# Kernel tuning notes

Measured on AMD Instinct MI355X. Metric: run time of the kernel, lower is better.

## Reference

```python
import jax, jax.numpy as jnp
import numpy as np

IN_FEATURES = 4096
OUT_FEATURES = 11008
BLOCK_SIZE = 64
BITS = 4
RANGE_MAX = 2 ** (BITS - 1) - 1  # 7


def setup_inputs() -> dict:
    key = jax.random.key(0)
    k1, k2, k3, k4 = jax.random.split(key, 4)
    n_blocks = OUT_FEATURES * IN_FEATURES // BLOCK_SIZE
    x = jax.random.normal(k1, (4, 2048, IN_FEATURES), dtype=jnp.float32)
    # int4 codes in [-7, 7]; stored signed int. Use randint in [-7, 8).
    weight_quant = jax.random.randint(k2, (n_blocks, BLOCK_SIZE), -RANGE_MAX, RANGE_MAX + 1, dtype=jnp.int32)
    weight_absmax = jax.random.uniform(k3, (n_blocks, 1), dtype=jnp.float32, minval=1e-5, maxval=1.0)
    bias = jax.random.normal(k4, (OUT_FEATURES,), dtype=jnp.float32)
    return {"x": x, "weight_quant": weight_quant, "weight_absmax": weight_absmax, "bias": bias}


def reference(x, weight_quant, weight_absmax, bias):
    # Blockwise dequant: q/range_max * absmax per block, reshape to (out, in). padding=0.
    w = (weight_quant.astype(jnp.float32) / RANGE_MAX) * weight_absmax  # [n_blocks, block]
    w = w.reshape(OUT_FEATURES, IN_FEATURES)
    # F.linear: y = x @ W^T + b
    return jnp.einsum('bsi,oi->bso', x, w) + bias
```

## Files before the change

### kernel.cpp

```cpp
#include <hip/hip_runtime.h>


#define K_DIM 4096
#define N_DIM 11008
#define M_DIM 8192
#define NT_K 64
#define AB_OFF 98304

typedef _Float16 f16;
typedef _Float16 f16x8 __attribute__((ext_vector_type(8)));
typedef float f32x4 __attribute__((ext_vector_type(4)));
typedef float fv4 __attribute__((ext_vector_type(4)));
typedef int iv4 __attribute__((ext_vector_type(4)));

__device__ __forceinline__ void gload16(const void* g, void* lds) {
  __builtin_amdgcn_global_load_lds(
      (__attribute__((address_space(1))) void*)g,
      (__attribute__((address_space(3))) void*)lds,
      16, 0, 0);
}

__global__ __launch_bounds__(256) void prep_kernel(const float* __restrict__ x,
                                                   f16* __restrict__ xo, int n8x,
                                                   const int* __restrict__ q,
                                                   const float* __restrict__ amax,
                                                   f16* __restrict__ wo, int n8w) {
  int i = blockIdx.x * blockDim.x + threadIdx.x;
  if (i < n8x) {
    const fv4* xv = (const fv4*)x;
    fv4 a = __builtin_nontemporal_load(xv + 2 * (size_t)i);
    fv4 b = __builtin_nontemporal_load(xv + 2 * (size_t)i + 1);
    f16x8 o;
    o[0] = (f16)a.x; o[1] = (f16)a.y; o[2] = (f16)a.z; o[3] = (f16)a.w;
    o[4] = (f16)b.x; o[5] = (f16)b.y; o[6] = (f16)b.z; o[7] = (f16)b.w;
    *(f16x8*)(xo + (size_t)i * 8) = o;
  } else {
    int j = i - n8x;
    if (j >= n8w) return;
    const iv4* qv = (const iv4*)q;
    iv4 a = __builtin_nontemporal_load(qv + 2 * (size_t)j);
    iv4 b = __builtin_nontemporal_load(qv + 2 * (size_t)j + 1);
    float s = amax[j >> 3] * (1.0f / 7.0f);
    f16x8 o;
    o[0] = (f16)((float)a.x * s); o[1] = (f16)((float)a.y * s);
    o[2] = (f16)((float)a.z * s); o[3] = (f16)((float)a.w * s);
    o[4] = (f16)((float)b.x * s); o[5] = (f16)((float)b.y * s);
    o[6] = (f16)((float)b.z * s); o[7] = (f16)((float)b.w * s);
    *(f16x8*)(wo + (size_t)j * 8) = o;
  }
}

__global__ __launch_bounds__(512, 2) void gemm_f16_bt(const f16* __restrict__ A,
                                                      const f16* __restrict__ B,
                                                      const float* __restrict__ bias,
                                                      float* __restrict__ C) {
  __shared__ __align__(16) char lds[163840];

  const int tid = threadIdx.x;
  const int w = tid >> 6;
  const int l = tid & 63;
  const int wr = w >> 2;
  const int wc = w & 3;

  const int wg = blockIdx.x;
  const int swz = (wg & 7) * 172 + (wg >> 3);
  const int mt = swz / 43;
  const int nt = swz % 43;
  const int m0 = mt * 256;
  const int n0 = nt * 256;

  const int lr = l & 15;
  const int g = l >> 4;
  const int laneoff = ((lr >> 1) << 7) | (((((lr & 1) << 6) | (g << 4))) ^ (((lr >> 1) & 7) << 4));

  const char* Asrc[2];
  const char* Bsrc[2];
#pragma unroll
  for (int j = 0; j < 2; ++j) {
    const int u = ((j * 8 + w) << 10) + l * 16;
    const int r = u >> 7;
    const int cp = (u & 127) ^ ((r & 7) << 4);
    const int ra = 2 * r + (cp >> 6);
    const int kb = cp & 63;
    Asrc[j] = (const char*)A + (size_t)(m0 + ra) * (K_DIM * 2) + kb;
    Bsrc[j] = (const char*)B + (size_t)(n0 + ra) * (K_DIM * 2) + kb;
  }

  char* ldsc = (char*)lds;

#define STAGE_A(dst_off, koff)              \
  {                                         \
    char* d_ = ldsc + (dst_off) + w * 1024; \
    gload16(Asrc[0] + (koff), d_);          \
    gload16(Asrc[1] + (koff), d_ + 8192);   \
  }
#define STAGE_B(dst_off, koff)              \
  {                                         \
    char* d_ = ldsc + (dst_off) + w * 1024; \
    gload16(Bsrc[0] + (koff), d_);          \
    gload16(Bsrc[1] + (koff), d_ + 8192);   \
  }

  f32x4 acc[8][4];
#pragma unroll
  for (int i = 0; i < 8; ++i)
#pragma unroll
    for (int j = 0; j < 4; ++j) acc[i][j] = (f32x4){0.f, 0.f, 0.f, 0.f};

  STAGE_A(0, 0);
  STAGE_A(16384, 64);
  STAGE_B(AB_OFF, 0);
  STAGE_B(AB_OFF + 16384, 64);
  STAGE_A(32768, 128);
  STAGE_A(32768 + 16384, 192);
  STAGE_B(AB_OFF + 32768, 128);
  STAGE_B(AB_OFF + 32768 + 16384, 192);
  asm volatile("s_waitcnt vmcnt(8)" ::: "memory");
  __builtin_amdgcn_s_barrier();

  int ap = 0;
  int ap2 = 65536;

  for (int t = 0; t < NT_K; ++t) {
    const int p = t & 1;
    const int Bb = AB_OFF + p * 32768;
    const int t2 = (t + 2 < NT_K) ? (t + 2) : (NT_K - 1);
    const int k2 = t2 * 128;

    f16x8 bf[4];
    f16x8 af[4];
#pragma unroll
    for (int pi = 0; pi < 4; ++pi) {
      const int kk = pi >> 1;
      const int mh = pi & 1;

      if (mh == 0) {
#pragma unroll
        for (int ni = 0; ni < 4; ++ni)
          bf[ni] = *(const f16x8*)(ldsc + Bb + kk * 16384 + ((wc * 64 + ni * 16) << 6) + laneoff);
      }
#pragma unroll
      for (int mi = 0; mi < 4; ++mi)
        af[mi] = *(const f16x8*)(ldsc + ap + kk * 16384 +
                                 ((wr * 128 + mh * 64 + mi * 16) << 6) + laneoff);

      if (pi == 0) {
        STAGE_A(ap2, k2);
      } else if (pi == 1) {
        STAGE_A(ap2 + 16384, k2 + 64);
      } else if (pi == 2) {
        STAGE_B(Bb, k2);
      } else {
        STAGE_B(Bb + 16384, k2 + 64);
      }

      __builtin_amdgcn_s_barrier();
      __builtin_amdgcn_s_setprio(1);
#pragma unroll
      for (int mi = 0; mi < 4; ++mi)
#pragma unroll
        for (int ni = 0; ni < 4; ++ni)
          acc[mh * 4 + mi][ni] = __builtin_amdgcn_mfma_f32_16x16x32_f16(
              af[mi], bf[ni], acc[mh * 4 + mi][ni], 0, 0, 0);
      __builtin_amdgcn_s_setprio(0);
      if (pi == 3) asm volatile("s_waitcnt vmcnt(8)" ::: "memory");
      __builtin_amdgcn_s_barrier();
    }

    ap += 32768;  if (ap == AB_OFF) ap = 0;
    ap2 += 32768; if (ap2 == AB_OFF) ap2 = 0;
  }

  const int orow = g * 4;
  float bv[4];
#pragma unroll
  for (int ni = 0; ni < 4; ++ni) bv[ni] = bias[n0 + wc * 64 + ni * 16 + lr];
#pragma unroll
  for (int mi = 0; mi < 8; ++mi) {
    const int row = m0 + wr * 128 + mi * 16 + orow;
#pragma unroll
    for (int ni = 0; ni < 4; ++ni) {
      const size_t cb = (size_t)row * N_DIM + (n0 + wc * 64 + ni * 16 + lr);
#pragma unroll
      for (int j = 0; j < 4; ++j)
        __builtin_nontemporal_store(acc[mi][ni][j] + bv[ni], &C[cb + (size_t)j * N_DIM]);
    }
  }
#undef STAGE_A
#undef STAGE_B
}

extern "C" void kernel_launch(void* const* d_in, const int* in_sizes, int n_in,
                              void* d_out, int out_size, void* d_ws, size_t ws_size,
                              hipStream_t stream) {
  const float* x = (const float*)d_in[0];
  const int* wq = (const int*)d_in[1];
  const float* amax = (const float*)d_in[2];
  const float* bias = (const float*)d_in[3];
  float* out = (float*)d_out;

  f16* Xh = (f16*)d_ws;
  f16* Wh = (f16*)((char*)d_ws + (size_t)M_DIM * K_DIM * 2);

  {
    int n8x = M_DIM * K_DIM / 8;
    int n8w = N_DIM * K_DIM / 8;
    int nthr = n8x + n8w;
    prep_kernel<<<(nthr + 255) / 256, 256, 0, stream>>>(x, Xh, n8x, wq, amax, Wh, n8w);
  }
  {
    dim3 grid((M_DIM / 256) * (N_DIM / 256));
    gemm_f16_bt<<<grid, 512, 0, stream>>>(Xh, Wh, bias, out);
  }
}
```

Before: 769.2 us.

## Switch GEMM to 32x32x16 MFMA with 3-slot K-pipeline and register double-buffering

Rewrites the main GEMM loop to use 32x32x16 f16 MFMA instructions instead of 16x16x32, with a single 64-wide K step per iteration and a triple-buffered LDS ring (96KB instead of 160KB). Fragment loads for the next half-step are issued before the current MFMAs, so LDS reads overlap matrix math, and each iteration needs only one barrier instead of eight. Larger MFMA tiles cut the number of LDS fragment reads per FLOP. In exchange the prefetch distance is shorter in bytes, which makes the kernel more exposed to global-load latency, and the epilogue uses a different store pattern.

```diff
diff --git a/kernel.cpp b/kernel.cpp
--- a/kernel.cpp
+++ b/kernel.cpp
@@ -4,12 +4,11 @@
 #define K_DIM 4096
 #define N_DIM 11008
 #define M_DIM 8192
-#define NT_K 64
-#define AB_OFF 98304
+#define NT 128
 
 typedef _Float16 f16;
 typedef _Float16 f16x8 __attribute__((ext_vector_type(8)));
-typedef float f32x4 __attribute__((ext_vector_type(4)));
+typedef float f32x16 __attribute__((ext_vector_type(16)));
 typedef float fv4 __attribute__((ext_vector_type(4)));
 typedef int iv4 __attribute__((ext_vector_type(4)));
 
@@ -54,7 +53,7 @@
                                                       const f16* __restrict__ B,
                                                       const float* __restrict__ bias,
                                                       float* __restrict__ C) {
-  __shared__ __align__(16) char lds[163840];
+  __shared__ __align__(16) char lds[98304];
 
   const int tid = threadIdx.x;
   const int w = tid >> 6;
@@ -69,121 +68,127 @@
   const int m0 = mt * 256;
   const int n0 = nt * 256;
 
-  const int lr = l & 15;
-  const int g = l >> 4;
-  const int laneoff = ((lr >> 1) << 7) | (((((lr & 1) << 6) | (g << 4))) ^ (((lr >> 1) & 7) << 4));
-
-  const char* Asrc[2];
-  const char* Bsrc[2];
+  const int l31 = l & 31;
+  const int lbase = (l31 >> 1) << 7;
+  const int lxor = ((l31 >> 1) & 7) << 4;
+  const int lk = ((l & 1) << 6) | ((l >> 5) << 4);
+  const int lt0 = lk ^ lxor;
+  const int lt1 = (lk | 32) ^ lxor;
+
+  const char* AsrcP[2];
+  const char* BsrcP[2];
 #pragma unroll
   for (int j = 0; j < 2; ++j) {
-    const int u = ((j * 8 + w) << 10) + l * 16;
+    const int u = ((w + j * 8) << 10) + l * 16;
     const int r = u >> 7;
     const int cp = (u & 127) ^ ((r & 7) << 4);
     const int ra = 2 * r + (cp >> 6);
     const int kb = cp & 63;
-    Asrc[j] = (const char*)A + (size_t)(m0 + ra) * (K_DIM * 2) + kb;
-    Bsrc[j] = (const char*)B + (size_t)(n0 + ra) * (K_DIM * 2) + kb;
+    AsrcP[j] = (const char*)A + (size_t)(m0 + ra) * (K_DIM * 2) + kb;
+    BsrcP[j] = (const char*)B + (size_t)(n0 + ra) * (K_DIM * 2) + kb;
   }
 
   char* ldsc = (char*)lds;
 
-#define STAGE_A(dst_off, koff)              \
-  {                                         \
-    char* d_ = ldsc + (dst_off) + w * 1024; \
-    gload16(Asrc[0] + (koff), d_);          \
-    gload16(Asrc[1] + (koff), d_ + 8192);   \
-  }
-#define STAGE_B(dst_off, koff)              \
-  {                                         \
-    char* d_ = ldsc + (dst_off) + w * 1024; \
-    gload16(Bsrc[0] + (koff), d_);          \
-    gload16(Bsrc[1] + (koff), d_ + 8192);   \
-  }
-
-  f32x4 acc[8][4];
-#pragma unroll
-  for (int i = 0; i < 8; ++i)
-#pragma unroll
-    for (int j = 0; j < 4; ++j) acc[i][j] = (f32x4){0.f, 0.f, 0.f, 0.f};
+#define STAGE_A(slot, koff)                          \
+  {                                                  \
+    char* d_ = ldsc + (slot) + w * 1024;             \
+    gload16(AsrcP[0] + (koff), d_);                  \
+    gload16(AsrcP[1] + (koff), d_ + 8192);           \
+  }
+#define STAGE_B(slot, koff)                          \
+  {                                                  \
+    char* d_ = ldsc + (slot) + w * 1024;             \
+    gload16(BsrcP[0] + (koff), d_);                  \
+    gload16(BsrcP[1] + (koff), d_ + 8192);           \
+  }
+
+  f32x16 acc[4][2];
+#pragma unroll
+  for (int i = 0; i < 4; ++i)
+#pragma unroll
+    for (int j = 0; j < 2; ++j) acc[i][j] = (f32x16)0.f;
+
+  const int aW = wr * 8192;
+  const int bW = wc * 4096;
 
   STAGE_A(0, 0);
+  STAGE_B(49152, 0);
   STAGE_A(16384, 64);
-  STAGE_B(AB_OFF, 0);
-  STAGE_B(AB_OFF + 16384, 64);
-  STAGE_A(32768, 128);
-  STAGE_A(32768 + 16384, 192);
-  STAGE_B(AB_OFF + 32768, 128);
-  STAGE_B(AB_OFF + 32768 + 16384, 192);
-  asm volatile("s_waitcnt vmcnt(8)" ::: "memory");
+  STAGE_B(49152 + 16384, 64);
+  asm volatile("s_waitcnt vmcnt(4)" ::: "memory");
   __builtin_amdgcn_s_barrier();
 
-  int ap = 0;
-  int ap2 = 65536;
-
-  for (int t = 0; t < NT_K; ++t) {
-    const int p = t & 1;
-    const int Bb = AB_OFF + p * 32768;
-    const int t2 = (t + 2 < NT_K) ? (t + 2) : (NT_K - 1);
-    const int k2 = t2 * 128;
-
-    f16x8 bf[4];
-    f16x8 af[4];
-#pragma unroll
-    for (int pi = 0; pi < 4; ++pi) {
-      const int kk = pi >> 1;
-      const int mh = pi & 1;
-
-      if (mh == 0) {
-#pragma unroll
-        for (int ni = 0; ni < 4; ++ni)
-          bf[ni] = *(const f16x8*)(ldsc + Bb + kk * 16384 + ((wc * 64 + ni * 16) << 6) + laneoff);
+  int aCur = 0, aNxt = 16384, aNx2 = 32768;
+  int bCur = 49152, bNxt = 65536, bNx2 = 81920;
+
+  f16x8 afa[4], bfa[2], afb[4], bfb[2];
+#pragma unroll
+  for (int mf = 0; mf < 4; ++mf)
+    afa[mf] = *(const f16x8*)(ldsc + aCur + aW + mf * 2048 + lbase + lt0);
+#pragma unroll
+  for (int nf = 0; nf < 2; ++nf)
+    bfa[nf] = *(const f16x8*)(ldsc + bCur + bW + nf * 2048 + lbase + lt0);
+
+  for (int t = 0; t < NT; ++t) {
+    const int t2 = (t + 2 < NT) ? (t + 2) : (NT - 1);
+    const int k2 = t2 * 64;
+
+    STAGE_A(aNx2, k2);
+#pragma unroll
+    for (int mf = 0; mf < 4; ++mf)
+      afb[mf] = *(const f16x8*)(ldsc + aCur + aW + mf * 2048 + lbase + lt1);
+#pragma unroll
+    for (int nf = 0; nf < 2; ++nf)
+      bfb[nf] = *(const f16x8*)(ldsc + bCur + bW + nf * 2048 + lbase + lt1);
+    __builtin_amdgcn_s_setprio(1);
+#pragma unroll
+    for (int mf = 0; mf < 4; ++mf)
+#pragma unroll
+      for (int nf = 0; nf < 2; ++nf)
+        acc[mf][nf] = __builtin_amdgcn_mfma_f32_32x32x16_f16(afa[mf], bfa[nf], acc[mf][nf], 0, 0, 0);
+    __builtin_amdgcn_s_setprio(0);
+
+    STAGE_B(bNx2, k2);
+    asm volatile("s_waitcnt lgkmcnt(0)" ::: "memory");
+    asm volatile("s_waitcnt vmcnt(4)" ::: "memory");
+    __builtin_amdgcn_s_barrier();
+#pragma unroll
+    for (int mf = 0; mf < 4; ++mf)
+      afa[mf] = *(const f16x8*)(ldsc + aNxt + aW + mf * 2048 + lbase + lt0);
+#pragma unroll
+    for (int nf = 0; nf < 2; ++nf)
+      bfa[nf] = *(const f16x8*)(ldsc + bNxt + bW + nf * 2048 + lbase + lt0);
+    __builtin_amdgcn_s_setprio(1);
+#pragma unroll
+    for (int mf = 0; mf < 4; ++mf)
+#pragma unroll
+      for (int nf = 0; nf < 2; ++nf)
+        acc[mf][nf] = __builtin_amdgcn_mfma_f32_32x32x16_f16(afb[mf], bfb[nf], acc[mf][nf], 0, 0, 0);
+    __builtin_amdgcn_s_setprio(0);
+
+    const int ta = aCur; aCur = aNxt; aNxt = aNx2; aNx2 = ta;
+    const int tb = bCur; bCur = bNxt; bNxt = bNx2; bNx2 = tb;
+  }
+
+  const int rbase = 4 * (l >> 5);
+  float bv[2];
+#pragma unroll
+  for (int nf = 0; nf < 2; ++nf) bv[nf] = bias[n0 + wc * 64 + nf * 32 + l31];
+#pragma unroll
+  for (int mf = 0; mf < 4; ++mf) {
+#pragma unroll
+    for (int nf = 0; nf < 2; ++nf) {
+      const size_t col = n0 + wc * 64 + nf * 32 + l31;
+#pragma unroll
+      for (int q = 0; q < 4; ++q) {
+#pragma unroll
+        for (int j = 0; j < 4; ++j) {
+          const int row = m0 + wr * 128 + mf * 32 + rbase + 8 * q + j;
+          __builtin_nontemporal_store(acc[mf][nf][q * 4 + j] + bv[nf],
+                                      &C[(size_t)row * N_DIM + col]);
+        }
       }
-#pragma unroll
-      for (int mi = 0; mi < 4; ++mi)
-        af[mi] = *(const f16x8*)(ldsc + ap + kk * 16384 +
-                                 ((wr * 128 + mh * 64 + mi * 16) << 6) + laneoff);
-
-      if (pi == 0) {
-        STAGE_A(ap2, k2);
-      } else if (pi == 1) {
-        STAGE_A(ap2 + 16384, k2 + 64);
-      } else if (pi == 2) {
-        STAGE_B(Bb, k2);
-      } else {
-        STAGE_B(Bb + 16384, k2 + 64);
-      }
-
-      __builtin_amdgcn_s_barrier();
-      __builtin_amdgcn_s_setprio(1);
-#pragma unroll
-      for (int mi = 0; mi < 4; ++mi)
-#pragma unroll
-        for (int ni = 0; ni < 4; ++ni)
-          acc[mh * 4 + mi][ni] = __builtin_amdgcn_mfma_f32_16x16x32_f16(
-              af[mi], bf[ni], acc[mh * 4 + mi][ni], 0, 0, 0);
-      __builtin_amdgcn_s_setprio(0);
-      if (pi == 3) asm volatile("s_waitcnt vmcnt(8)" ::: "memory");
-      __builtin_amdgcn_s_barrier();
-    }
-
-    ap += 32768;  if (ap == AB_OFF) ap = 0;
-    ap2 += 32768; if (ap2 == AB_OFF) ap2 = 0;
-  }
-
-  const int orow = g * 4;
-  float bv[4];
-#pragma unroll
-  for (int ni = 0; ni < 4; ++ni) bv[ni] = bias[n0 + wc * 64 + ni * 16 + lr];
-#pragma unroll
-  for (int mi = 0; mi < 8; ++mi) {
-    const int row = m0 + wr * 128 + mi * 16 + orow;
-#pragma unroll
-    for (int ni = 0; ni < 4; ++ni) {
-      const size_t cb = (size_t)row * N_DIM + (n0 + wc * 64 + ni * 16 + lr);
-#pragma unroll
-      for (int j = 0; j < 4; ++j)
-        __builtin_nontemporal_store(acc[mi][ni][j] + bv[ni], &C[cb + (size_t)j * N_DIM]);
     }
   }
 #undef STAGE_A
```

Result: slower. 839.7 us (+9.2%).

## Switch GEMM inner loop to 32x32x16 MFMA tiles with re-staged prefetch order

Applied to the files above, without the earlier changes.

Replaces the 16x16x32 MFMA accumulation with 32x32x16 MFMA instructions, changing the per-wave fragment layout (4x2 tiles of 32x32), the LDS read offsets and the epilogue row/column mapping. Larger MFMA tiles reduce the number of LDS fragment reads per FLOP and the instruction count. The global-to-LDS prefetch schedule is also reordered so part of the next B tile loads one iteration later, with vmcnt waits adjusted to 6, and an explicit lgkmcnt wait plus sched_barrier is added before the MFMA block. The reordered staging risks correctness or stalls if the wait counts do not match outstanding loads.

```diff
diff --git a/kernel.cpp b/kernel.cpp
--- a/kernel.cpp
+++ b/kernel.cpp
@@ -9,7 +9,7 @@
 
 typedef _Float16 f16;
 typedef _Float16 f16x8 __attribute__((ext_vector_type(8)));
-typedef float f32x4 __attribute__((ext_vector_type(4)));
+typedef float f32x16 __attribute__((ext_vector_type(16)));
 typedef float fv4 __attribute__((ext_vector_type(4)));
 typedef int iv4 __attribute__((ext_vector_type(4)));
 
@@ -69,21 +69,24 @@
   const int m0 = mt * 256;
   const int n0 = nt * 256;
 
-  const int lr = l & 15;
-  const int g = l >> 4;
-  const int laneoff = ((lr >> 1) << 7) | (((((lr & 1) << 6) | (g << 4))) ^ (((lr >> 1) & 7) << 4));
-
-  const char* Asrc[2];
-  const char* Bsrc[2];
+  const int l31 = l & 31;
+  const int lbase = (l31 >> 1) << 7;
+  const int lxor = ((l31 >> 1) & 7) << 4;
+  const int lk0 = ((l & 1) << 6) | ((l >> 5) << 4);
+  const int lt0 = lk0 ^ lxor;
+  const int lt1 = (lk0 | 32) ^ lxor;
+
+  const char* AsrcP[2];
+  const char* BsrcP[2];
 #pragma unroll
   for (int j = 0; j < 2; ++j) {
-    const int u = ((j * 8 + w) << 10) + l * 16;
+    const int u = ((w + j * 8) << 10) + l * 16;
     const int r = u >> 7;
     const int cp = (u & 127) ^ ((r & 7) << 4);
     const int ra = 2 * r + (cp >> 6);
     const int kb = cp & 63;
-    Asrc[j] = (const char*)A + (size_t)(m0 + ra) * (K_DIM * 2) + kb;
-    Bsrc[j] = (const char*)B + (size_t)(n0 + ra) * (K_DIM * 2) + kb;
+    AsrcP[j] = (const char*)A + (size_t)(m0 + ra) * (K_DIM * 2) + kb;
+    BsrcP[j] = (const char*)B + (size_t)(n0 + ra) * (K_DIM * 2) + kb;
   }
 
   char* ldsc = (char*)lds;
@@ -91,21 +94,24 @@
 #define STAGE_A(dst_off, koff)              \
   {                                         \
     char* d_ = ldsc + (dst_off) + w * 1024; \
-    gload16(Asrc[0] + (koff), d_);          \
-    gload16(Asrc[1] + (koff), d_ + 8192);   \
+    gload16(AsrcP[0] + (koff), d_);         \
+    gload16(AsrcP[1] + (koff), d_ + 8192);  \
   }
 #define STAGE_B(dst_off, koff)              \
   {                                         \
     char* d_ = ldsc + (dst_off) + w * 1024; \
-    gload16(Bsrc[0] + (koff), d_);          \
-    gload16(Bsrc[1] + (koff), d_ + 8192);   \
-  }
-
-  f32x4 acc[8][4];
-#pragma unroll
-  for (int i = 0; i < 8; ++i)
-#pragma unroll
-    for (int j = 0; j < 4; ++j) acc[i][j] = (f32x4){0.f, 0.f, 0.f, 0.f};
+    gload16(BsrcP[0] + (koff), d_);         \
+    gload16(BsrcP[1] + (koff), d_ + 8192);  \
+  }
+
+  f32x16 acc[4][2];
+#pragma unroll
+  for (int i = 0; i < 4; ++i)
+#pragma unroll
+    for (int j = 0; j < 2; ++j) acc[i][j] = (f32x16)0.f;
+
+  const int aW = wr * 8192;
+  const int bW = wc * 4096;
 
   STAGE_A(0, 0);
   STAGE_A(16384, 64);
@@ -114,8 +120,7 @@
   STAGE_A(32768, 128);
   STAGE_A(32768 + 16384, 192);
   STAGE_B(AB_OFF + 32768, 128);
-  STAGE_B(AB_OFF + 32768 + 16384, 192);
-  asm volatile("s_waitcnt vmcnt(8)" ::: "memory");
+  asm volatile("s_waitcnt vmcnt(6)" ::: "memory");
   __builtin_amdgcn_s_barrier();
 
   int ap = 0;
@@ -123,47 +128,48 @@
 
   for (int t = 0; t < NT_K; ++t) {
     const int p = t & 1;
+    const int pn = p ^ 1;
     const int Bb = AB_OFF + p * 32768;
+    const int Bn = AB_OFF + pn * 32768;
+    const int t1 = (t + 1 < NT_K) ? (t + 1) : (NT_K - 1);
     const int t2 = (t + 2 < NT_K) ? (t + 2) : (NT_K - 1);
+    const int k1 = t1 * 128;
     const int k2 = t2 * 128;
 
-    f16x8 bf[4];
-    f16x8 af[4];
 #pragma unroll
     for (int pi = 0; pi < 4; ++pi) {
       const int kk = pi >> 1;
-      const int mh = pi & 1;
-
-      if (mh == 0) {
-#pragma unroll
-        for (int ni = 0; ni < 4; ++ni)
-          bf[ni] = *(const f16x8*)(ldsc + Bb + kk * 16384 + ((wc * 64 + ni * 16) << 6) + laneoff);
+      const int kt = (pi & 1) ? lt1 : lt0;
+
+      f16x8 af[4], bf[2];
+#pragma unroll
+      for (int mf = 0; mf < 4; ++mf)
+        af[mf] = *(const f16x8*)(ldsc + ap + kk * 16384 + aW + mf * 2048 + lbase + kt);
+#pragma unroll
+      for (int nf = 0; nf < 2; ++nf)
+        bf[nf] = *(const f16x8*)(ldsc + Bb + kk * 16384 + bW + nf * 2048 + lbase + kt);
+
+      if (pi == 0) {
+        STAGE_B(Bn + 16384, k1 + 64);
+      } else if (pi == 1) {
+        STAGE_A(ap2, k2);
+      } else if (pi == 2) {
+        STAGE_A(ap2 + 16384, k2 + 64);
+      } else {
+        STAGE_B(Bb, k2);
       }
-#pragma unroll
-      for (int mi = 0; mi < 4; ++mi)
-        af[mi] = *(const f16x8*)(ldsc + ap + kk * 16384 +
-                                 ((wr * 128 + mh * 64 + mi * 16) << 6) + laneoff);
-
-      if (pi == 0) {
-        STAGE_A(ap2, k2);
-      } else if (pi == 1) {
-        STAGE_A(ap2 + 16384, k2 + 64);
-      } else if (pi == 2) {
-        STAGE_B(Bb, k2);
-      } else {
-        STAGE_B(Bb + 16384, k2 + 64);
-      }
 
       __builtin_amdgcn_s_barrier();
+      asm volatile("s_waitcnt lgkmcnt(0)" ::: "memory");
+      __builtin_amdgcn_sched_barrier(0);
       __builtin_amdgcn_s_setprio(1);
 #pragma unroll
-      for (int mi = 0; mi < 4; ++mi)
-#pragma unroll
-        for (int ni = 0; ni < 4; ++ni)
-          acc[mh * 4 + mi][ni] = __builtin_amdgcn_mfma_f32_16x16x32_f16(
-              af[mi], bf[ni], acc[mh * 4 + mi][ni], 0, 0, 0);
+      for (int mf = 0; mf < 4; ++mf)
+#pragma unroll
+        for (int nf = 0; nf < 2; ++nf)
+          acc[mf][nf] = __builtin_amdgcn_mfma_f32_32x32x16_f16(af[mf], bf[nf], acc[mf][nf], 0, 0, 0);
       __builtin_amdgcn_s_setprio(0);
-      if (pi == 3) asm volatile("s_waitcnt vmcnt(8)" ::: "memory");
+      if (pi == 3) asm volatile("s_waitcnt vmcnt(6)" ::: "memory");
       __builtin_amdgcn_s_barrier();
     }
 
@@ -171,19 +177,24 @@
     ap2 += 32768; if (ap2 == AB_OFF) ap2 = 0;
   }
 
-  const int orow = g * 4;
-  float bv[4];
-#pragma unroll
-  for (int ni = 0; ni < 4; ++ni) bv[ni] = bias[n0 + wc * 64 + ni * 16 + lr];
-#pragma unroll
-  for (int mi = 0; mi < 8; ++mi) {
-    const int row = m0 + wr * 128 + mi * 16 + orow;
-#pragma unroll
-    for (int ni = 0; ni < 4; ++ni) {
-      const size_t cb = (size_t)row * N_DIM + (n0 + wc * 64 + ni * 16 + lr);
-#pragma unroll
-      for (int j = 0; j < 4; ++j)
-        __builtin_nontemporal_store(acc[mi][ni][j] + bv[ni], &C[cb + (size_t)j * N_DIM]);
+  const int rbase = 4 * (l >> 5);
+  float bv[2];
+#pragma unroll
+  for (int nf = 0; nf < 2; ++nf) bv[nf] = bias[n0 + wc * 64 + nf * 32 + l31];
+#pragma unroll
+  for (int mf = 0; mf < 4; ++mf) {
+#pragma unroll
+    for (int nf = 0; nf < 2; ++nf) {
+      const size_t col = n0 + wc * 64 + nf * 32 + l31;
+#pragma unroll
+      for (int q = 0; q < 4; ++q) {
+#pragma unroll
+        for (int j = 0; j < 4; ++j) {
+          const int row = m0 + wr * 128 + mf * 32 + rbase + 8 * q + j;
+          __builtin_nontemporal_store(acc[mf][nf][q * 4 + j] + bv[nf],
+                                      &C[(size_t)row * N_DIM + col]);
+        }
+      }
     }
   }
 #undef STAGE_A
```

New measurement: 855.6 us. 11.2% more time.
